# Performance work log

Measured on AMD Instinct MI355X. Metric: run time of the kernel, lower is better.

The kernel has to match this reference:

```python
import jax, jax.numpy as jnp
import numpy as np

B, A, C, M = 8, 98304, 80, 32
ALPHA, GAMMA = 0.25, 2.0


def setup_inputs() -> dict:
    key = jax.random.key(0)
    k1, k2, k3, k4, k5, k6, k7, k8 = jax.random.split(key, 8)
    classifications = jax.random.uniform(k1, (B, A, C), dtype=jnp.float32)
    regressions = jax.random.normal(k2, (B, A, 4), dtype=jnp.float32)
    # valid anchor boxes inside a 640px image
    ax = jax.random.uniform(k3, (A,)) * 512.0
    ay = jax.random.uniform(k4, (A,)) * 512.0
    aw = jax.random.uniform(k5, (A, 2)) * 120.0 + 8.0
    anchors = jnp.stack([ax, ay, ax + aw[:, 0], ay + aw[:, 1]], axis=-1)[None].astype(jnp.float32)
    # valid GT boxes with class labels in [0, C) (no -1 padding: all annotations valid)
    gx = jax.random.uniform(k6, (B, M, 2)) * 480.0
    gw = jax.random.uniform(k7, (B, M, 2)) * 150.0 + 10.0
    gcls = jax.random.randint(k8, (B, M), 0, C).astype(jnp.float32)
    annotations = jnp.concatenate([gx, gx + gw, gcls[..., None]], axis=-1).astype(jnp.float32)
    return {
        "classifications": classifications,
        "regressions": regressions,
        "anchors": anchors,
        "annotations": annotations,
        "negative_iou_thr": 0.4,
        "positive_iou_thr": 0.5,
    }


def calc_iou(a, b):
    # a: [A,4] anchors, b: [M,4] gt boxes -> [A,M]
    area = (b[:, 2] - b[:, 0]) * (b[:, 3] - b[:, 1])
    iw = jnp.clip(jnp.minimum(a[:, 2:3], b[:, 2]) - jnp.maximum(a[:, 0:1], b[:, 0]), 0.0)
    ih = jnp.clip(jnp.minimum(a[:, 3:4], b[:, 3]) - jnp.maximum(a[:, 1:2], b[:, 1]), 0.0)
    inter = iw * ih
    ua = jnp.clip(((a[:, 2] - a[:, 0]) * (a[:, 3] - a[:, 1]))[:, None] + area - inter, 1e-8)
    return inter / ua


def focal_loss(classifications, regressions, anchors, annotations, negative_iou_thr, positive_iou_thr):
    anchor = anchors[0]  # [A,4]
    aw = anchor[:, 2] - anchor[:, 0]
    ah = anchor[:, 3] - anchor[:, 1]
    acx = anchor[:, 0] + 0.5 * aw
    acy = anchor[:, 1] + 0.5 * ah

    def per_image(classification, regression, annot):
        p = jnp.clip(classification, 1e-4, 1.0 - 1e-4)
        valid = annot[:, 4] != -1.0  # [M] (all valid in test data)
        iou = jnp.where(valid[None, :], calc_iou(anchor, annot[:, :4]), -1.0)  # [A,M]
        iou_max = jnp.max(iou, axis=1)
        iou_arg = jnp.argmax(iou, axis=1)
        assigned = annot[iou_arg]  # [A,5]

        pos = iou_max >= positive_iou_thr  # [A]
        num_pos = jnp.sum(pos.astype(jnp.float32))
        onehot = jax.nn.one_hot(assigned[:, 4].astype(jnp.int32), C, dtype=jnp.float32)
        # targets: 1 for assigned class on positives, 0 elsewhere on pos/neg anchors, -1 ignored
        targets = jnp.where(pos[:, None], onehot,
                            jnp.where((iou_max < negative_iou_thr)[:, None], 0.0, -1.0))

        is_one = targets == 1.0
        alpha_factor = jnp.where(is_one, ALPHA, 1.0 - ALPHA)
        focal_w = alpha_factor * jnp.where(is_one, 1.0 - p, p) ** GAMMA
        bce = -(targets * jnp.log(p) + (1.0 - targets) * jnp.log(1.0 - p))
        cls_loss = jnp.where(targets != -1.0, focal_w * bce, 0.0)
        cls_loss = jnp.sum(cls_loss) / jnp.clip(num_pos, 1.0)

        gw = jnp.clip(assigned[:, 2] - assigned[:, 0], None, None)
        gh = assigned[:, 3] - assigned[:, 1]
        gcx = assigned[:, 0] + 0.5 * gw
        gcy = assigned[:, 1] + 0.5 * gh
        gw = jnp.clip(gw, 1.0)
        gh = jnp.clip(gh, 1.0)
        t = jnp.stack([(gcx - acx) / aw, (gcy - acy) / ah,
                       jnp.log(gw / aw), jnp.log(gh / ah)], axis=1)
        t = t / jnp.array([0.1, 0.1, 0.2, 0.2], dtype=jnp.float32)
        diff = jnp.abs(t - regression)
        sl1 = jnp.where(diff <= 1.0 / 9.0, 0.5 * 9.0 * diff * diff, diff - 0.5 / 9.0)
        reg_loss = jnp.sum(jnp.where(pos[:, None], sl1, 0.0)) / jnp.clip(num_pos * 4.0, 1.0)
        return cls_loss, reg_loss

    cls_l, reg_l = jax.vmap(per_image)(classifications, regressions, annotations)
    return jnp.mean(cls_l).reshape(1), jnp.mean(reg_l).reshape(1)


def reference(classifications, regressions, anchors, annotations, negative_iou_thr, positive_iou_thr):
    return focal_loss(classifications, regressions, anchors, annotations,
                      negative_iou_thr, positive_iou_thr)
```

## Files before the change

### kernel.cpp

```cpp
#include <hip/hip_runtime.h>

#define B_ 8
#define A_ 98304
#define C_ 80
#define M_ 32
#define BLK 256
#define ITERS 20
#define NWAVE (BLK / 64)
#define TILES_PER_IMG (A_ / BLK)
#define NTILES (B_ * TILES_PER_IMG)
#define GRID 1536

typedef float vfloat4 __attribute__((ext_vector_type(4)));

#define NEGC (-0.75f * 0.69314718055994531f)

__device__ __forceinline__ float neg_u(float praw) {
    const float p = fminf(praw, 1.0f - 1e-4f);
    return p * p * __log2f(1.0f - p);
}

__device__ __forceinline__ float smooth_l1(float t, float r) {
    float d = fabsf(t - r);
    return (d <= (1.0f / 9.0f)) ? (0.5f * 9.0f * d * d) : (d - 0.5f / 9.0f);
}

__global__ __launch_bounds__(BLK) void focal_main(
    const float* __restrict__ cls,
    const float* __restrict__ regr,
    const float* __restrict__ anchors,
    const float* __restrict__ ann,
    const float* __restrict__ neg_thr_p,
    const float* __restrict__ pos_thr_p,
    float* __restrict__ acc)
{
    __shared__ float s_x0[M_], s_y0[M_], s_x1[M_], s_y1[M_], s_ab[M_], s_cls[M_];
    __shared__ float s_w[BLK];
    __shared__ float s_red[NWAVE * 3];

    const int tid = threadIdx.x;
    const float neg_thr = neg_thr_p[0];
    const float pos_thr = pos_thr_p[0];

    for (int t = blockIdx.x; t < NTILES; t += GRID) {
        const int b  = t / TILES_PER_IMG;
        const int a0 = (t % TILES_PER_IMG) * BLK;

        if (tid < M_) {
            const float* am = ann + ((size_t)b * M_ + tid) * 5;
            const float x0 = am[0], y0 = am[1], x1 = am[2], y1 = am[3], cl = am[4];
            s_x0[tid] = x0; s_y0[tid] = y0; s_x1[tid] = x1; s_y1[tid] = y1;
            s_ab[tid] = (x1 - x0) * (y1 - y0);
            s_cls[tid] = cl;
        }
        __syncthreads();

        const int a = a0 + tid;
        const float4 an = reinterpret_cast<const float4*>(anchors)[a];
        const float aw = an.z - an.x;
        const float ah = an.w - an.y;
        const float areaA = aw * ah;

        float ib = -1.0f, ub = 1.0f;
        int   arg = 0;
#pragma unroll
        for (int m = 0; m < M_; ++m) {
            const float iw = fmaxf(fminf(an.z, s_x1[m]) - fmaxf(an.x, s_x0[m]), 0.0f);
            const float ih = fmaxf(fminf(an.w, s_y1[m]) - fmaxf(an.y, s_y0[m]), 0.0f);
            float inter = iw * ih;
            const float ua = fmaxf(areaA + s_ab[m] - inter, 1e-8f);
            if (s_cls[m] == -1.0f) inter = -1.0f;
            if (inter * ub > ib * ua) { ib = inter; ub = ua; arg = m; }
        }
        const bool pos = (ib >= pos_thr * ub);
        const bool neg = (ib <  neg_thr * ub);

        float reg_partial = 0.0f;
        float pos_count   = 0.0f;
        float cls_corr    = 0.0f;

        if (pos) {
            pos_count = 1.0f;
            const float gx0 = s_x0[arg], gy0 = s_y0[arg];
            const float gx1 = s_x1[arg], gy1 = s_y1[arg];
            const int   kcls = (int)s_cls[arg];

            float gw = gx1 - gx0;
            float gh = gy1 - gy0;
            const float gcx = gx0 + 0.5f * gw;
            const float gcy = gy0 + 0.5f * gh;
            gw = fmaxf(gw, 1.0f);
            gh = fmaxf(gh, 1.0f);
            const float acx = an.x + 0.5f * aw;
            const float acy = an.y + 0.5f * ah;
            const float t0 = ((gcx - acx) / aw) * 10.0f;
            const float t1 = ((gcy - acy) / ah) * 10.0f;
            const float t2 = logf(gw / aw) * 5.0f;
            const float t3 = logf(gh / ah) * 5.0f;
            const vfloat4 r = __builtin_nontemporal_load(
                &reinterpret_cast<const vfloat4*>(regr)[(size_t)b * A_ + a]);
            reg_partial = smooth_l1(t0, r.x) + smooth_l1(t1, r.y) +
                          smooth_l1(t2, r.z) + smooth_l1(t3, r.w);

            const float praw = cls[((size_t)b * A_ + a) * C_ + kcls];
            const float p  = fminf(fmaxf(praw, 1e-4f), 1.0f - 1e-4f);
            const float om = 1.0f - p;
            const float negv = neg_u(praw) * NEGC;
            const float posv = 0.25f * om * om * (-__logf(p));
            cls_corr = posv - negv;
        }
        s_w[tid] = (pos || neg) ? NEGC : 0.0f;
        __syncthreads();

        const vfloat4* tile4 = reinterpret_cast<const vfloat4*>(
            cls + ((size_t)b * A_ + a0) * C_);
        float s0 = 0.0f, s1 = 0.0f;
#pragma unroll 5
        for (int it = 0; it < ITERS; ++it) {
            const int vid = it * BLK + tid;
            const vfloat4 v = __builtin_nontemporal_load(&tile4[vid]);
            const float cw = s_w[(unsigned)vid / 20u];
            s0 = fmaf(neg_u(v.x) + neg_u(v.y), cw, s0);
            s1 = fmaf(neg_u(v.z) + neg_u(v.w), cw, s1);
        }
        float cls_partial = cls_corr + s0 + s1;

#pragma unroll
        for (int off = 32; off > 0; off >>= 1) {
            cls_partial += __shfl_down(cls_partial, off);
            reg_partial += __shfl_down(reg_partial, off);
            pos_count   += __shfl_down(pos_count,   off);
        }
        const int wave = tid >> 6;
        if ((tid & 63) == 0) {
            s_red[wave * 3 + 0] = cls_partial;
            s_red[wave * 3 + 1] = reg_partial;
            s_red[wave * 3 + 2] = pos_count;
        }
        __syncthreads();
        if (tid == 0) {
            float c = 0.0f, r = 0.0f, n = 0.0f;
#pragma unroll
            for (int wv = 0; wv < NWAVE; ++wv) {
                c += s_red[wv * 3 + 0];
                r += s_red[wv * 3 + 1];
                n += s_red[wv * 3 + 2];
            }
            atomicAdd(&acc[b * 3 + 0], c);
            atomicAdd(&acc[b * 3 + 1], r);
            atomicAdd(&acc[b * 3 + 2], n);
        }
        __syncthreads();
    }
}

__global__ void focal_finalize(const float* __restrict__ acc, float* __restrict__ out) {
    const int t = threadIdx.x;
    float cls_l = 0.0f, reg_l = 0.0f;
    if (t < B_) {
        const float np = acc[t * 3 + 2];
        cls_l = acc[t * 3 + 0] / fmaxf(np, 1.0f);
        reg_l = acc[t * 3 + 1] / fmaxf(np * 4.0f, 1.0f);
    }
#pragma unroll
    for (int off = 32; off > 0; off >>= 1) {
        cls_l += __shfl_down(cls_l, off);
        reg_l += __shfl_down(reg_l, off);
    }
    if (t == 0) {
        out[0] = cls_l / (float)B_;
        out[1] = reg_l / (float)B_;
    }
}

extern "C" void kernel_launch(void* const* d_in, const int* in_sizes, int n_in,
                              void* d_out, int out_size, void* d_ws, size_t ws_size,
                              hipStream_t stream) {
    const float* cls     = (const float*)d_in[0];
    const float* regr    = (const float*)d_in[1];
    const float* anchors = (const float*)d_in[2];
    const float* ann     = (const float*)d_in[3];
    const float* negt    = (const float*)d_in[4];
    const float* post    = (const float*)d_in[5];
    float* acc = (float*)d_ws;

    (void)hipMemsetAsync(acc, 0, B_ * 3 * sizeof(float), stream);
    focal_main<<<GRID, BLK, 0, stream>>>(cls, regr, anchors, ann,
                                         negt, post, acc);
    focal_finalize<<<1, 64, 0, stream>>>(acc, (float*)d_out);
}
```

Measured before the change: 117.6 us.

## Double-buffer classification tiles into LDS via async global_load_lds

The classification stream is now staged through two shared-memory buffers using the hardware global-to-LDS load builtin. The next chunk, or the first chunk of the block's next tile, is prefetched while the current chunk is reduced. The grid shrinks so each block processes exactly three tiles in a fixed loop, and the regression load becomes an ordinary cached load. This aims to hide global-memory latency in a bandwidth-bound reduction, at the cost of extra LDS use, a barrier per chunk, and reliance on the barrier to order completion of the asynchronous loads.

Result: slower. 121.6 us (+3.5%).

```diff
diff --git a/kernel.cpp b/kernel.cpp
--- a/kernel.cpp
+++ b/kernel.cpp
@@ -1,19 +1,21 @@
 #include <hip/hip_runtime.h>
+#include <stdint.h>
 
 #define B_ 8
 #define A_ 98304
 #define C_ 80
 #define M_ 32
 #define BLK 256
-#define ITERS 20
 #define NWAVE (BLK / 64)
 #define TILES_PER_IMG (A_ / BLK)
 #define NTILES (B_ * TILES_PER_IMG)
-#define GRID 1536
+#define GRID 1024
+#define TPB (NTILES / GRID)
+#define CHUNK_F4 1024
+#define CHUNKS 5
+#define NEGC (-0.75f * 0.69314718055994531f)
 
 typedef float vfloat4 __attribute__((ext_vector_type(4)));
-
-#define NEGC (-0.75f * 0.69314718055994531f)
 
 __device__ __forceinline__ float neg_u(float praw) {
     const float p = fminf(praw, 1.0f - 1e-4f);
@@ -23,6 +25,14 @@
 __device__ __forceinline__ float smooth_l1(float t, float r) {
     float d = fabsf(t - r);
     return (d <= (1.0f / 9.0f)) ? (0.5f * 9.0f * d * d) : (d - 0.5f / 9.0f);
+}
+
+__device__ __forceinline__ void stage16(const void* g, void* l) {
+    auto gp = reinterpret_cast<__attribute__((address_space(1))) void*>(
+        reinterpret_cast<uintptr_t>(g));
+    auto lp = reinterpret_cast<__attribute__((address_space(3))) void*>(
+        (uint32_t)reinterpret_cast<uintptr_t>(l));
+    __builtin_amdgcn_global_load_lds(gp, lp, 16, 0, 0);
 }
 
 __global__ __launch_bounds__(BLK) void focal_main(
@@ -34,6 +44,7 @@
     const float* __restrict__ pos_thr_p,
     float* __restrict__ acc)
 {
+    __shared__ vfloat4 s_buf[2][CHUNK_F4];
     __shared__ float s_x0[M_], s_y0[M_], s_x1[M_], s_y1[M_], s_ab[M_], s_cls[M_];
     __shared__ float s_w[BLK];
     __shared__ float s_red[NWAVE * 3];
@@ -42,9 +53,24 @@
     const float neg_thr = neg_thr_p[0];
     const float pos_thr = pos_thr_p[0];
 
-    for (int t = blockIdx.x; t < NTILES; t += GRID) {
-        const int b  = t / TILES_PER_IMG;
-        const int a0 = (t % TILES_PER_IMG) * BLK;
+    auto stage_chunk = [&](int tgl, int c, int nb) {
+        const int bb  = tgl / TILES_PER_IMG;
+        const int aa0 = (tgl % TILES_PER_IMG) * BLK;
+        const vfloat4* tb = reinterpret_cast<const vfloat4*>(
+            cls + ((size_t)bb * A_ + aa0) * C_);
+#pragma unroll
+        for (int k = 0; k < 4; ++k)
+            stage16(&tb[c * CHUNK_F4 + k * BLK + tid],
+                    &s_buf[nb][k * BLK + (tid & 192)]);
+    };
+
+    int pb = 0;
+    stage_chunk(blockIdx.x, 0, 0);
+
+    for (int tq = 0; tq < TPB; ++tq) {
+        const int tgl = blockIdx.x + tq * GRID;
+        const int b   = tgl / TILES_PER_IMG;
+        const int a0  = (tgl % TILES_PER_IMG) * BLK;
 
         if (tid < M_) {
             const float* am = ann + ((size_t)b * M_ + tid) * 5;
@@ -97,31 +123,32 @@
             const float t1 = ((gcy - acy) / ah) * 10.0f;
             const float t2 = logf(gw / aw) * 5.0f;
             const float t3 = logf(gh / ah) * 5.0f;
-            const vfloat4 r = __builtin_nontemporal_load(
-                &reinterpret_cast<const vfloat4*>(regr)[(size_t)b * A_ + a]);
+            const float4 r = reinterpret_cast<const float4*>(regr)[(size_t)b * A_ + a];
             reg_partial = smooth_l1(t0, r.x) + smooth_l1(t1, r.y) +
                           smooth_l1(t2, r.z) + smooth_l1(t3, r.w);
 
             const float praw = cls[((size_t)b * A_ + a) * C_ + kcls];
             const float p  = fminf(fmaxf(praw, 1e-4f), 1.0f - 1e-4f);
             const float om = 1.0f - p;
-            const float negv = neg_u(praw) * NEGC;
-            const float posv = 0.25f * om * om * (-__logf(p));
-            cls_corr = posv - negv;
+            cls_corr = 0.25f * om * om * (-__logf(p)) - neg_u(praw) * NEGC;
         }
         s_w[tid] = (pos || neg) ? NEGC : 0.0f;
         __syncthreads();
 
-        const vfloat4* tile4 = reinterpret_cast<const vfloat4*>(
-            cls + ((size_t)b * A_ + a0) * C_);
         float s0 = 0.0f, s1 = 0.0f;
-#pragma unroll 5
-        for (int it = 0; it < ITERS; ++it) {
-            const int vid = it * BLK + tid;
-            const vfloat4 v = __builtin_nontemporal_load(&tile4[vid]);
-            const float cw = s_w[(unsigned)vid / 20u];
-            s0 = fmaf(neg_u(v.x) + neg_u(v.y), cw, s0);
-            s1 = fmaf(neg_u(v.z) + neg_u(v.w), cw, s1);
+        for (int c = 0; c < CHUNKS; ++c) {
+            if (c + 1 < CHUNKS)            stage_chunk(tgl, c + 1, pb ^ 1);
+            else if (tq + 1 < TPB)         stage_chunk(blockIdx.x + (tq + 1) * GRID, 0, pb ^ 1);
+#pragma unroll
+            for (int j = 0; j < 4; ++j) {
+                const vfloat4 v = s_buf[pb][j * BLK + tid];
+                const unsigned f4i = (unsigned)(c * CHUNK_F4 + j * BLK + tid);
+                const float cw = s_w[f4i / 20u];
+                s0 = fmaf(neg_u(v.x) + neg_u(v.y), cw, s0);
+                s1 = fmaf(neg_u(v.z) + neg_u(v.w), cw, s1);
+            }
+            __syncthreads();
+            pb ^= 1;
         }
         float cls_partial = cls_corr + s0 + s1;
 
@@ -150,7 +177,6 @@
             atomicAdd(&acc[b * 3 + 1], r);
             atomicAdd(&acc[b * 3 + 2], n);
         }
-        __syncthreads();
     }
 }
 
```
